# Kernel tuning notes

Measured on AMD Instinct MI355X. Metric: run time of the kernel, lower is better.

The kernel has to match this reference:

```python
import jax, jax.numpy as jnp
import numpy as np

B, N, T, OBS, ACT, M, EMB = 128, 128, 256, 512, 64, 16, 128
H = T // 2  # bi-LSTM hidden per direction
EPS = 1e-5


def _ln(x, g, b):
    mu = x.mean(-1, keepdims=True)
    var = ((x - mu) ** 2).mean(-1, keepdims=True)
    return (x - mu) / jnp.sqrt(var + EPS) * g + b


def _lstm_dir(xs, Wih, Whh, bih, bhh):
    # xs: [m, T] -> hidden states [m, H]; torch gate order i,f,g,o
    h0 = jnp.zeros(xs.shape[:-2] + (H,), xs.dtype)

    def cell(carry, x):
        h, c = carry
        z = x @ Wih.T + h @ Whh.T + bih + bhh
        i, f, g, o = jnp.split(z, 4, axis=-1)
        c = jax.nn.sigmoid(f) * c + jax.nn.sigmoid(i) * jnp.tanh(g)
        h = jax.nn.sigmoid(o) * jnp.tanh(c)
        return (h, c), h

    (_, _), hs = jax.lax.scan(cell, (h0, h0), xs)
    return hs


def setup_inputs() -> dict:
    key = jax.random.key(0)
    ks = iter(jax.random.split(key, 32))

    def lin(fi, shape):
        return jax.random.normal(next(ks), shape, jnp.float32) / float(np.sqrt(fi))

    z = lambda *s: jnp.zeros(s, jnp.float32)
    o = lambda *s: jnp.ones(s, jnp.float32)
    return dict(
        obs=jax.random.normal(next(ks), (B, N, OBS), jnp.float32),
        W1=lin(OBS, (OBS, T)), b1=z(T), g1=o(T), be1=z(T),
        W2=lin(T, (T, T)), b2=z(T), g2=o(T), be2=z(T),
        Wa1=lin(T, (T, EMB)), ba1=z(EMB),
        Wa2=lin(EMB, (EMB, EMB)), ba2=z(EMB),
        Wa3=lin(EMB, (EMB, 1)), ba3=z(1),
        Wf_ih=lin(T, (4 * H, T)), Wf_hh=lin(H, (4 * H, H)), bf_ih=z(4 * H), bf_hh=z(4 * H),
        Wb_ih=lin(T, (4 * H, T)), Wb_hh=lin(H, (4 * H, H)), bb_ih=z(4 * H), bb_hh=z(4 * H),
        W3=lin(T, (T, T)), b3=z(T), g3=o(T), be3=z(T),
        W4=lin(T, (T, ACT)), b4=z(ACT), g4=o(ACT), be4=z(ACT),
    )


def reference(obs, W1, b1, g1, be1, W2, b2, g2, be2,
              Wa1, ba1, Wa2, ba2, Wa3, ba3,
              Wf_ih, Wf_hh, bf_ih, bf_hh, Wb_ih, Wb_hh, bb_ih, bb_hh,
              W3, b3, g3, be3, W4, b4, g4, be4):
    # actor_1: Linear -> LN -> ReLU -> Linear -> LN
    h = jax.nn.relu(_ln(obs @ W1 + b1, g1, be1))
    thoughts = _ln(h @ W2 + b2, g2, be2)              # [B,N,T]

    # attention unit: 2-layer MLP + sigmoid
    a = jax.nn.relu(thoughts @ Wa1 + ba1)
    a = jax.nn.relu(a @ Wa2 + ba2)
    init_prob = jax.nn.sigmoid(a @ Wa3 + ba3)          # [B,N,1]
    is_init = init_prob[..., 0] > 0.4                  # [B,N]

    # pairwise squared distances via bmm (same expansion as torch code)
    dot = jnp.einsum('bit,bjt->bij', thoughts, thoughts)
    sq = jnp.diagonal(dot, axis1=1, axis2=2)           # [B,N]
    dists = sq[:, None, :] - 2.0 * dot + sq[:, :, None]

    # top-m nearest neighbors per agent, then agent-index order (matches j-loop order)
    _, idx = jax.lax.top_k(-dists, M)                  # [B,N,M]
    idx = jnp.sort(idx, axis=-1)

    bidx = jnp.arange(B)[:, None, None]
    aidx = jnp.arange(N)[None, :, None]
    C = jnp.zeros((B, N, N), thoughts.dtype).at[bidx, aidx, idx].set(1.0)
    C = C * is_init[..., None].astype(thoughts.dtype)

    old_thoughts = thoughts

    # sequential per-agent communication: gather group, bi-LSTM, scatter back
    def update_one(th, grp_idx, flags):
        def step(t, inp):
            gi, fl = inp
            grp = t[gi]                                 # [M,T]
            hf = _lstm_dir(grp, Wf_ih, Wf_hh, bf_ih, bf_hh)
            hb = _lstm_dir(grp[::-1], Wb_ih, Wb_hh, bb_ih, bb_hh)[::-1]
            integ = jnp.concatenate([hf, hb], -1)       # [M,T]
            t = t.at[gi].set(jnp.where(fl, integ, grp))
            return t, None
        t, _ = jax.lax.scan(step, th, (grp_idx, flags))
        return t

    new_thoughts = jax.vmap(update_one)(thoughts, idx, is_init)

    # actor_2: ReLU -> Linear -> LN -> Linear -> LN -> Tanh
    h2 = jax.nn.relu(new_thoughts)
    h2 = _ln(h2 @ W3 + b3, g3, be3)
    acts = jnp.tanh(_ln(h2 @ W4 + b4, g4, be4))
    return acts, C, init_prob, is_init, new_thoughts, old_thoughts
```

## Files before the change

kernel.cpp:

```cpp
#include <hip/hip_runtime.h>
#include <math.h>

typedef __attribute__((ext_vector_type(8))) short bf16x8;
typedef __attribute__((ext_vector_type(4))) float f32x4;

__device__ __forceinline__ unsigned short f2bf(float x) {
    unsigned int u = __float_as_uint(x);
    u += 0x7fffu + ((u >> 16) & 1u);
    return (unsigned short)(u >> 16);
}
__device__ __forceinline__ float bf2f(unsigned short b) {
    return __uint_as_float(((unsigned int)b) << 16);
}
__device__ __forceinline__ float fsig(float z) {
    float e = __expf(-z);
    return __builtin_amdgcn_rcpf(1.f + e);
}
__device__ __forceinline__ float ftanh(float x) {
    float e = __expf(-2.f * x);
    float s = __builtin_amdgcn_rcpf(1.f + e);
    return fmaf(2.f, s, -1.f);
}
__device__ __forceinline__ bf16x8 pack8(float4 a, float4 b) {
    bf16x8 r;
    r[0] = (short)f2bf(a.x); r[1] = (short)f2bf(a.y);
    r[2] = (short)f2bf(a.z); r[3] = (short)f2bf(a.w);
    r[4] = (short)f2bf(b.x); r[5] = (short)f2bf(b.y);
    r[6] = (short)f2bf(b.z); r[7] = (short)f2bf(b.w);
    return r;
}

__global__ void prep_kernel(const float* __restrict__ Wf_ih, const float* __restrict__ Wb_ih,
                            const float* __restrict__ Wf_hh, const float* __restrict__ Wb_hh,
                            const float* __restrict__ bf_ih, const float* __restrict__ bf_hh,
                            const float* __restrict__ bb_ih, const float* __restrict__ bb_hh,
                            unsigned short* __restrict__ wihbf,
                            unsigned short* __restrict__ whhbf,
                            float* __restrict__ biasz) {
    int i = blockIdx.x * 256 + threadIdx.x;
    if (i < 131072) {
        wihbf[i]          = f2bf(Wf_ih[i]);
        wihbf[131072 + i] = f2bf(Wb_ih[i]);
    }
    if (i < 65536) {
        whhbf[i]         = f2bf(Wf_hh[i]);
        whhbf[65536 + i] = f2bf(Wb_hh[i]);
    }
    if (i < 512) {
        biasz[i]       = bf_ih[i] + bf_hh[i];
        biasz[512 + i] = bb_ih[i] + bb_hh[i];
    }
}

__global__ __launch_bounds__(256) void gemm64(const float* __restrict__ A,
                                              const float* __restrict__ Bm,
                                              const float* __restrict__ bias,
                                              float* __restrict__ C,
                                              int M, int N, int K, int flags) {
    __shared__ float As[16][68];
    __shared__ float Bs[16][68];
    const int t = threadIdx.x;
    const int row0 = blockIdx.y * 64, col0 = blockIdx.x * 64;
    const int tm = t >> 4, tn = t & 15;
    float acc[4][4] = {};
    for (int k0 = 0; k0 < K; k0 += 16) {
        {
            int r = t >> 2, kq = (t & 3) * 4;
            float4 v = *(const float4*)(A + (size_t)(row0 + r) * K + k0 + kq);
            if (flags & 2) {
                v.x = fmaxf(v.x, 0.f); v.y = fmaxf(v.y, 0.f);
                v.z = fmaxf(v.z, 0.f); v.w = fmaxf(v.w, 0.f);
            }
            As[kq + 0][r] = v.x; As[kq + 1][r] = v.y;
            As[kq + 2][r] = v.z; As[kq + 3][r] = v.w;
        }
        {
            int kk = t >> 4, nq = (t & 15) * 4;
            float4 v = *(const float4*)(Bm + (size_t)(k0 + kk) * N + col0 + nq);
            *(float4*)&Bs[kk][nq] = v;
        }
        __syncthreads();
#pragma unroll
        for (int kk = 0; kk < 16; ++kk) {
            float a[4], b[4];
#pragma unroll
            for (int i = 0; i < 4; ++i) a[i] = As[kk][tm * 4 + i];
#pragma unroll
            for (int j = 0; j < 4; ++j) b[j] = Bs[kk][tn * 4 + j];
#pragma unroll
            for (int i = 0; i < 4; ++i)
#pragma unroll
                for (int j = 0; j < 4; ++j) acc[i][j] = fmaf(a[i], b[j], acc[i][j]);
        }
        __syncthreads();
    }
#pragma unroll
    for (int i = 0; i < 4; ++i) {
#pragma unroll
        for (int j = 0; j < 4; ++j) {
            int col = col0 + tn * 4 + j;
            float v = acc[i][j] + (bias ? bias[col] : 0.f);
            if (flags & 1) v = fmaxf(v, 0.f);
            C[(size_t)(row0 + tm * 4 + i) * N + col] = v;
        }
    }
}

__global__ __launch_bounds__(256) void ln256_kernel(const float* __restrict__ X,
                                                    float* __restrict__ Y,
                                                    float* __restrict__ Y2,
                                                    const float* __restrict__ gam,
                                                    const float* __restrict__ bet,
                                                    int relu) {
#pragma clang fp contract(off)
    int row = blockIdx.x * 4 + (threadIdx.x >> 6);
    int l = threadIdx.x & 63;
    float4 x = *(const float4*)(X + (size_t)row * 256 + l * 4);
    float s = x.x + x.y + x.z + x.w;
#pragma unroll
    for (int d = 1; d < 64; d <<= 1) s += __shfl_xor(s, d);
    float mu = s * (1.f / 256.f);
    float d0 = x.x - mu, d1 = x.y - mu, d2 = x.z - mu, d3 = x.w - mu;
    float ss = d0 * d0 + d1 * d1 + d2 * d2 + d3 * d3;
#pragma unroll
    for (int d = 1; d < 64; d <<= 1) ss += __shfl_xor(ss, d);
    float var = ss * (1.f / 256.f);
    float sd = sqrtf(var + 1e-5f);
    float4 y;
    y.x = (d0 / sd) * gam[l * 4 + 0] + bet[l * 4 + 0];
    y.y = (d1 / sd) * gam[l * 4 + 1] + bet[l * 4 + 1];
    y.z = (d2 / sd) * gam[l * 4 + 2] + bet[l * 4 + 2];
    y.w = (d3 / sd) * gam[l * 4 + 3] + bet[l * 4 + 3];
    if (relu) {
        y.x = fmaxf(y.x, 0.f); y.y = fmaxf(y.y, 0.f);
        y.z = fmaxf(y.z, 0.f); y.w = fmaxf(y.w, 0.f);
    }
    *(float4*)(Y + (size_t)row * 256 + l * 4) = y;
    if (Y2) *(float4*)(Y2 + (size_t)row * 256 + l * 4) = y;
}

__global__ __launch_bounds__(256) void ln64_tanh_kernel(const float* __restrict__ X,
                                                        float* __restrict__ Y,
                                                        const float* __restrict__ gam,
                                                        const float* __restrict__ bet) {
#pragma clang fp contract(off)
    int row = blockIdx.x * 4 + (threadIdx.x >> 6);
    int l = threadIdx.x & 63;
    float x = X[(size_t)row * 64 + l];
    float s = x;
#pragma unroll
    for (int d = 1; d < 64; d <<= 1) s += __shfl_xor(s, d);
    float mu = s * (1.f / 64.f);
    float dx = x - mu;
    float ss = dx * dx;
#pragma unroll
    for (int d = 1; d < 64; d <<= 1) ss += __shfl_xor(ss, d);
    float var = ss * (1.f / 64.f);
    float sd = sqrtf(var + 1e-5f);
    float y = tanhf((dx / sd) * gam[l] + bet[l]);
    Y[(size_t)row * 64 + l] = y;
}

__global__ __launch_bounds__(256) void attn_head_kernel(const float* __restrict__ a2,
                                                        const float* __restrict__ Wa3,
                                                        const float* __restrict__ ba3,
                                                        float* __restrict__ outP,
                                                        float* __restrict__ outInit,
                                                        int* __restrict__ flags) {
#pragma clang fp contract(off)
    int row = blockIdx.x * 4 + (threadIdx.x >> 6);
    int l = threadIdx.x & 63;
    float s = a2[(size_t)row * 128 + l] * Wa3[l] + a2[(size_t)row * 128 + 64 + l] * Wa3[64 + l];
#pragma unroll
    for (int d = 1; d < 64; d <<= 1) s += __shfl_xor(s, d);
    s += ba3[0];
    float p = 1.f / (1.f + expf(-s));
    if (l == 0) {
        outP[row] = p;
        int f = (p > 0.4f) ? 1 : 0;
        outInit[row] = f ? 1.f : 0.f;
        flags[row] = f;
    }
}

__global__ __launch_bounds__(256) void dot_kernel(const float* __restrict__ th,
                                                  float* __restrict__ dotm) {
    __shared__ float As[16][68];
    __shared__ float Bs[16][132];
    const int b = blockIdx.x >> 1, half = blockIdx.x & 1;
    const int t = threadIdx.x;
    const int tm = t >> 4, tn = t & 15;
    float acc[4][8] = {};
    const float* base = th + (size_t)b * 128 * 256;
    for (int k0 = 0; k0 < 256; k0 += 16) {
        {
            int r = t >> 2, kq = (t & 3) * 4;
            float4 v = *(const float4*)(base + (size_t)(half * 64 + r) * 256 + k0 + kq);
            As[kq + 0][r] = v.x; As[kq + 1][r] = v.y;
            As[kq + 2][r] = v.z; As[kq + 3][r] = v.w;
        }
        {
            int n = t >> 1, kq = (t & 1) * 8;
            const float* src = base + (size_t)n * 256 + k0 + kq;
            float4 v0 = *(const float4*)src;
            float4 v1 = *(const float4*)(src + 4);
            Bs[kq + 0][n] = v0.x; Bs[kq + 1][n] = v0.y;
            Bs[kq + 2][n] = v0.z; Bs[kq + 3][n] = v0.w;
            Bs[kq + 4][n] = v1.x; Bs[kq + 5][n] = v1.y;
            Bs[kq + 6][n] = v1.z; Bs[kq + 7][n] = v1.w;
        }
        __syncthreads();
#pragma unroll
        for (int kk = 0; kk < 16; ++kk) {
            float a[4], bb[8];
#pragma unroll
            for (int i = 0; i < 4; ++i) a[i] = As[kk][tm * 4 + i];
#pragma unroll
            for (int j = 0; j < 8; ++j) bb[j] = Bs[kk][tn * 8 + j];
#pragma unroll
            for (int i = 0; i < 4; ++i)
#pragma unroll
                for (int j = 0; j < 8; ++j) acc[i][j] = fmaf(a[i], bb[j], acc[i][j]);
        }
        __syncthreads();
    }
#pragma unroll
    for (int i = 0; i < 4; ++i)
#pragma unroll
        for (int j = 0; j < 8; ++j)
            dotm[(size_t)b * 16384 + (size_t)(half * 64 + tm * 4 + i) * 128 + tn * 8 + j] = acc[i][j];
}

__global__ void sq_kernel(const float* __restrict__ dotm, float* __restrict__ sq) {
    int i = blockIdx.x * 256 + threadIdx.x;
    int b = i >> 7, n = i & 127;
    sq[i] = dotm[(size_t)b * 16384 + (size_t)n * 129];
}

__global__ __launch_bounds__(256) void topk_kernel(const float* __restrict__ dotm,
                                                   const float* __restrict__ sq,
                                                   const int* __restrict__ flags,
                                                   float* __restrict__ outC,
                                                   int* __restrict__ idxb) {
#pragma clang fp contract(off)
    int row = blockIdx.x * 4 + (threadIdx.x >> 6);
    int l = threadIdx.x & 63;
    int b = row >> 7;
    const float* drow = dotm + (size_t)row * 128;
    float sqi = sq[row];
    float t0 = 2.f * drow[l];
    float v0 = sq[b * 128 + l] - t0; v0 = v0 + sqi;
    float t1 = 2.f * drow[64 + l];
    float v1 = sq[b * 128 + 64 + l] - t1; v1 = v1 + sqi;

    unsigned long long mlo = 0ull, mhi = 0ull;
#pragma unroll 1
    for (int n = 0; n < 16; ++n) {
        float bv = v0; int bi = l;
        if (v1 < bv) { bv = v1; bi = 64 + l; }
#pragma unroll
        for (int d = 1; d < 64; d <<= 1) {
            float ov = __shfl_xor(bv, d);
            int oi = __shfl_xor(bi, d);
            if (ov < bv || (ov == bv && oi < bi)) { bv = ov; bi = oi; }
        }
        if (bi < 64) mlo |= (1ull << bi); else mhi |= (1ull << (bi - 64));
        if (l == bi) v0 = __builtin_inff();
        if (64 + l == bi) v1 = __builtin_inff();
    }
    float fl = (flags[row] != 0) ? 1.f : 0.f;
    outC[(size_t)row * 128 + l]      = fl * (((mlo >> l) & 1ull) ? 1.f : 0.f);
    outC[(size_t)row * 128 + 64 + l] = fl * (((mhi >> l) & 1ull) ? 1.f : 0.f);
    if (l < 16) {
        int cnt = 0, found = -1;
        for (int jj = 0; jj < 128; ++jj) {
            bool bit = (jj < 64) ? ((mlo >> jj) & 1ull) : ((mhi >> (jj - 64)) & 1ull);
            if (bit) { if (cnt == l) { found = jj; break; } ++cnt; }
        }
        idxb[(size_t)row * 16 + l] = found;
    }
}

__global__ __launch_bounds__(512, 2) void chain_kernel(float* __restrict__ th,
                                                       const unsigned short* __restrict__ whhbf,
                                                       const unsigned short* __restrict__ wihbf,
                                                       const float* __restrict__ biasz,
                                                       const int* __restrict__ idxb,
                                                       const int* __restrict__ flags) {
    const int b = blockIdx.x;
    const int t = threadIdx.x;
    const int l = t & 63, lr = l & 15, lg = l >> 4;
    const int w = t >> 6, dir = w >> 2, wd = w & 3;

    __shared__ __align__(16) unsigned short thl[128 * 256];
    __shared__ __align__(16) unsigned short xgs2[2 * 4 * 16 * 16 * 8];
    __shared__ __align__(16) unsigned short hsnap[2][18][128];
    __shared__ int idxl[2048];
    __shared__ int flg[128];

    {
        int r = t >> 2, c0 = (t & 3) * 64;
        const float* src = th + (size_t)(b * 128 + r) * 256 + c0;
        char* rowb = (char*)thl + r * 512;
        int swz = (r & 7) << 4;
#pragma unroll
        for (int i = 0; i < 8; ++i) {
            float4 v0 = *(const float4*)(src + i * 8);
            float4 v1 = *(const float4*)(src + i * 8 + 4);
            *(bf16x8*)(rowb + (((c0 + i * 8) * 2) ^ swz)) = pack8(v0, v1);
        }
    }
    if (t < 128) flg[t] = flags[b * 128 + t];
    if (t < 256) {
        int d2 = t >> 7, j = t & 127;
        hsnap[d2][0][j] = 0;
        hsnap[d2][17][j] = 0;
    }
#pragma unroll
    for (int c = 0; c < 4; ++c) idxl[t + c * 512] = idxb[(size_t)b * 2048 + c * 512 + t];

    bf16x8 wf[4][2][4];
    {
        const unsigned short* whh = whhbf + (size_t)dir * 65536;
#pragma unroll
        for (int G = 0; G < 4; ++G)
#pragma unroll
            for (int hf = 0; hf < 2; ++hf) {
                int gate = G * 128 + wd * 32 + 2 * lr + hf;
#pragma unroll
                for (int kc = 0; kc < 4; ++kc)
                    wf[G][hf][kc] = *(const bf16x8*)(whh + (size_t)gate * 128 + kc * 32 + lg * 8);
            }
    }
    const unsigned short* wih = wihbf + (size_t)dir * 131072;
    float bzr[8];
#pragma unroll
    for (int tt = 0; tt < 8; ++tt)
        bzr[tt] = biasz[dir * 512 + (tt >> 1) * 128 + wd * 32 + 2 * lr + (tt & 1)];
    __syncthreads();

    for (int ag = 0; ag < 128; ++ag) {
        if (!flg[ag]) continue;
        const int gi_lr = idxl[ag * 16 + lr];
        const int xgbase = ((dir * 4 + wd) * 16) * 16 * 8;

        {
            f32x4 xa[8];
#pragma unroll
            for (int tt = 0; tt < 8; ++tt) xa[tt] = (f32x4){0.f, 0.f, 0.f, 0.f};
            const char* arow = (const char*)thl + gi_lr * 512;
            const int aswz = (gi_lr & 7) << 4;
#pragma unroll
            for (int kc = 0; kc < 8; ++kc) {
                bf16x8 af = *(const bf16x8*)(arow + ((kc * 64 + lg * 16) ^ aswz));
#pragma unroll
                for (int tt = 0; tt < 8; ++tt) {
                    const unsigned short* wb =
                        wih + (size_t)((tt >> 1) * 128 + wd * 32 + 2 * lr + (tt & 1)) * 256 +
                        kc * 32 + lg * 8;
                    xa[tt] = __builtin_amdgcn_mfma_f32_16x16x32_bf16(
                        af, *(const bf16x8*)wb, xa[tt], 0, 0, 0);
                }
            }
#pragma unroll
            for (int r = 0; r < 4; ++r) {
                bf16x8 pk;
#pragma unroll
                for (int tt = 0; tt < 8; ++tt) pk[tt] = (short)f2bf(xa[tt][r] + bzr[tt]);
                int m = lg * 4 + r;
                *(bf16x8*)&xgs2[xgbase + (m * 16 + lr) * 8] = pk;
            }
        }
        __syncthreads();

        bf16x8 xpn = *(const bf16x8*)&xgs2[xgbase + ((dir ? 15 : 0) * 16 + lr) * 8];

        float cst0 = 0.f, cst1 = 0.f;
        for (int s = 0; s < 16; ++s) {
            const int m = dir ? (15 - s) : s;
            const int rprev = dir ? (m + 2) : m;
            f32x4 acc[4][2];
#pragma unroll
            for (int G = 0; G < 4; ++G) {
                acc[G][0] = (f32x4){0.f, 0.f, 0.f, 0.f};
                acc[G][1] = (f32x4){0.f, 0.f, 0.f, 0.f};
            }
#pragma unroll
            for (int kc = 0; kc < 4; ++kc) {
                bf16x8 ha = *(const bf16x8*)(&hsnap[dir][rprev][kc * 32 + lg * 8]);
#pragma unroll
                for (int G = 0; G < 4; ++G) {
                    acc[G][0] = __builtin_amdgcn_mfma_f32_16x16x32_bf16(
                        ha, wf[G][0][kc], acc[G][0], 0, 0, 0);
                    acc[G][1] = __builtin_amdgcn_mfma_f32_16x16x32_bf16(
                        ha, wf[G][1][kc], acc[G][1], 0, 0, 0);
                }
            }
            bf16x8 xp = xpn;
            float zi0 = acc[0][0][0] + bf2f((unsigned short)xp[0]);
            float zi1 = acc[0][1][0] + bf2f((unsigned short)xp[1]);
            float zf0 = acc[1][0][0] + bf2f((unsigned short)xp[2]);
            float zf1 = acc[1][1][0] + bf2f((unsigned short)xp[3]);
            float zg0 = acc[2][0][0] + bf2f((unsigned short)xp[4]);
            float zg1 = acc[2][1][0] + bf2f((unsigned short)xp[5]);
            float zo0 = acc[3][0][0] + bf2f((unsigned short)xp[6]);
            float zo1 = acc[3][1][0] + bf2f((unsigned short)xp[7]);
            float i0 = fsig(zi0), f0 = fsig(zf0), g0 = ftanh(zg0), o0 = fsig(zo0);
            cst0 = f0 * cst0 + i0 * g0;
            float h0 = o0 * ftanh(cst0);
            float i1 = fsig(zi1), f1 = fsig(zf1), g1 = ftanh(zg1), o1 = fsig(zo1);
            cst1 = f1 * cst1 + i1 * g1;
            float h1 = o1 * ftanh(cst1);
            if (lg == 0) {
                unsigned int hw = (unsigned int)f2bf(h0) | ((unsigned int)f2bf(h1) << 16);
                *(unsigned int*)&hsnap[dir][m + 1][wd * 32 + 2 * lr] = hw;
            }
            if (s < 15) {
                int mn = dir ? (14 - s) : (s + 1);
                xpn = *(const bf16x8*)&xgs2[xgbase + (mn * 16 + lr) * 8];
            }
            __syncthreads();
        }

        {
            int d2 = t >> 8, m = (t >> 4) & 15, c8 = (t & 15) * 8;
            bf16x8 v = *(const bf16x8*)&hsnap[d2][m + 1][c8];
            int row = idxl[ag * 16 + m];
            *(bf16x8*)((char*)thl + row * 512 + (((d2 * 128 + c8) * 2) ^ ((row & 7) << 4))) = v;
        }
        __syncthreads();
    }

    {
        int r = t >> 2, c0 = (t & 3) * 64;
        const char* rowb = (const char*)thl + r * 512;
        int swz = (r & 7) << 4;
        float* dst = th + (size_t)(b * 128 + r) * 256 + c0;
#pragma unroll
        for (int i = 0; i < 8; ++i) {
            bf16x8 sv = *(const bf16x8*)(rowb + (((c0 + i * 8) * 2) ^ swz));
            float4 v0, v1;
            v0.x = bf2f((unsigned short)sv[0]); v0.y = bf2f((unsigned short)sv[1]);
            v0.z = bf2f((unsigned short)sv[2]); v0.w = bf2f((unsigned short)sv[3]);
            v1.x = bf2f((unsigned short)sv[4]); v1.y = bf2f((unsigned short)sv[5]);
            v1.z = bf2f((unsigned short)sv[6]); v1.w = bf2f((unsigned short)sv[7]);
            *(float4*)(dst + i * 8) = v0;
            *(float4*)(dst + i * 8 + 4) = v1;
        }
    }
}

extern "C" void kernel_launch(void* const* d_in, const int* in_sizes, int n_in,
                              void* d_out, int out_size, void* d_ws, size_t ws_size,
                              hipStream_t stream) {
    const float* obs  = (const float*)d_in[0];
    const float* W1   = (const float*)d_in[1];
    const float* b1   = (const float*)d_in[2];
    const float* gg1  = (const float*)d_in[3];
    const float* be1  = (const float*)d_in[4];
    const float* W2   = (const float*)d_in[5];
    const float* b2   = (const float*)d_in[6];
    const float* gg2  = (const float*)d_in[7];
    const float* be2  = (const float*)d_in[8];
    const float* Wa1  = (const float*)d_in[9];
    const float* ba1  = (const float*)d_in[10];
    const float* Wa2  = (const float*)d_in[11];
    const float* ba2  = (const float*)d_in[12];
    const float* Wa3  = (const float*)d_in[13];
    const float* ba3  = (const float*)d_in[14];
    const float* Wf_ih = (const float*)d_in[15];
    const float* Wf_hh = (const float*)d_in[16];
    const float* bf_ih = (const float*)d_in[17];
    const float* bf_hh = (const float*)d_in[18];
    const float* Wb_ih = (const float*)d_in[19];
    const float* Wb_hh = (const float*)d_in[20];
    const float* bb_ih = (const float*)d_in[21];
    const float* bb_hh = (const float*)d_in[22];
    const float* W3   = (const float*)d_in[23];
    const float* b3   = (const float*)d_in[24];
    const float* gg3  = (const float*)d_in[25];
    const float* be3  = (const float*)d_in[26];
    const float* W4   = (const float*)d_in[27];
    const float* b4   = (const float*)d_in[28];
    const float* gg4  = (const float*)d_in[29];
    const float* be4  = (const float*)d_in[30];

    float* out     = (float*)d_out;
    float* out_acts = out;
    float* out_C    = out + 1048576;
    float* out_ip   = out + 3145728;
    float* out_ii   = out + 3162112;
    float* out_nt   = out + 3178496;
    float* out_ot   = out + 7372800;

    float* ws    = (float*)d_ws;
    float* h1    = ws;
    float* abuf  = ws + 4194304;
    float* a2buf = ws + 6291456;
    unsigned short* wihbf = (unsigned short*)(ws + 8388608);
    float* biasz = ws + 8519680;
    unsigned short* whhbf = (unsigned short*)(ws + 8520704);
    float* sqb   = ws + 8586240;
    int* idxb    = (int*)(ws + 8602624);
    int* flagsb  = (int*)(ws + 8864768);

    prep_kernel<<<512, 256, 0, stream>>>(Wf_ih, Wb_ih, Wf_hh, Wb_hh,
                                         bf_ih, bf_hh, bb_ih, bb_hh,
                                         wihbf, whhbf, biasz);

    gemm64<<<dim3(4, 256), 256, 0, stream>>>(obs, W1, b1, h1, 16384, 256, 512, 0);
    ln256_kernel<<<4096, 256, 0, stream>>>(h1, h1, nullptr, gg1, be1, 1);
    gemm64<<<dim3(4, 256), 256, 0, stream>>>(h1, W2, b2, out_nt, 16384, 256, 256, 0);
    ln256_kernel<<<4096, 256, 0, stream>>>(out_nt, out_nt, out_ot, gg2, be2, 0);

    gemm64<<<dim3(2, 256), 256, 0, stream>>>(out_nt, Wa1, ba1, abuf, 16384, 128, 256, 1);
    gemm64<<<dim3(2, 256), 256, 0, stream>>>(abuf, Wa2, ba2, a2buf, 16384, 128, 128, 1);
    attn_head_kernel<<<4096, 256, 0, stream>>>(a2buf, Wa3, ba3, out_ip, out_ii, flagsb);

    dot_kernel<<<256, 256, 0, stream>>>(out_nt, abuf);
    sq_kernel<<<64, 256, 0, stream>>>(abuf, sqb);
    topk_kernel<<<4096, 256, 0, stream>>>(abuf, sqb, flagsb, out_C, idxb);

    chain_kernel<<<128, 512, 0, stream>>>(out_nt, whhbf, wihbf, biasz, idxb, flagsb);

    gemm64<<<dim3(4, 256), 256, 0, stream>>>(out_nt, W3, b3, h1, 16384, 256, 256, 2);
    ln256_kernel<<<4096, 256, 0, stream>>>(h1, h1, nullptr, gg3, be3, 0);
    gemm64<<<dim3(1, 256), 256, 0, stream>>>(h1, W4, b4, a2buf, 16384, 64, 256, 0);
    ln64_tanh_kernel<<<4096, 256, 0, stream>>>(a2buf, out_acts, gg4, be4);
}
```

Baseline: 3.612 ms.

## Interleave two batches per chain block and move thought state to global bf16

The chain kernel now processes two batch elements per workgroup, running 64 blocks instead of 128. The two independent LSTM recurrences are interleaved so their MFMA and transcendental latencies can overlap. The per-batch thought matrix no longer lives in LDS. A separate kernel converts it to a global bf16 copy, which is read for the input projection and written back together with fp32 updates. The biases and input gates are folded into the accumulator initialisation. The trade-off is half as many blocks, which halves the parallelism across CUs, plus global-memory latency on the gather path.

Result: slower. 7.664 ms (+112.2%).

```diff
diff --git a/kernel.cpp b/kernel.cpp
--- a/kernel.cpp
+++ b/kernel.cpp
@@ -50,6 +50,13 @@
         biasz[i]       = bf_ih[i] + bf_hh[i];
         biasz[512 + i] = bb_ih[i] + bb_hh[i];
     }
+}
+
+__global__ void tobf_kernel(const float* __restrict__ x, unsigned short* __restrict__ y) {
+    int i = (blockIdx.x * 256 + threadIdx.x) * 8;
+    float4 v0 = *(const float4*)(x + i);
+    float4 v1 = *(const float4*)(x + i + 4);
+    *(bf16x8*)(y + i) = pack8(v0, v1);
 }
 
 __global__ __launch_bounds__(256) void gemm64(const float* __restrict__ A,
@@ -282,42 +289,36 @@
 }
 
 __global__ __launch_bounds__(512, 2) void chain_kernel(float* __restrict__ th,
+                                                       unsigned short* __restrict__ thbf,
                                                        const unsigned short* __restrict__ whhbf,
                                                        const unsigned short* __restrict__ wihbf,
                                                        const float* __restrict__ biasz,
                                                        const int* __restrict__ idxb,
                                                        const int* __restrict__ flags) {
-    const int b = blockIdx.x;
+    const int blk = blockIdx.x;
     const int t = threadIdx.x;
     const int l = t & 63, lr = l & 15, lg = l >> 4;
     const int w = t >> 6, dir = w >> 2, wd = w & 3;
 
-    __shared__ __align__(16) unsigned short thl[128 * 256];
-    __shared__ __align__(16) unsigned short xgs2[2 * 4 * 16 * 16 * 8];
-    __shared__ __align__(16) unsigned short hsnap[2][18][128];
-    __shared__ int idxl[2048];
-    __shared__ int flg[128];
-
-    {
-        int r = t >> 2, c0 = (t & 3) * 64;
-        const float* src = th + (size_t)(b * 128 + r) * 256 + c0;
-        char* rowb = (char*)thl + r * 512;
-        int swz = (r & 7) << 4;
-#pragma unroll
-        for (int i = 0; i < 8; ++i) {
-            float4 v0 = *(const float4*)(src + i * 8);
-            float4 v1 = *(const float4*)(src + i * 8 + 4);
-            *(bf16x8*)(rowb + (((c0 + i * 8) * 2) ^ swz)) = pack8(v0, v1);
-        }
-    }
-    if (t < 128) flg[t] = flags[b * 128 + t];
+    __shared__ __align__(16) unsigned short xgs2[2][16384];
+    __shared__ __align__(16) unsigned short hsnap[2][2][18][128];
+    __shared__ int idxl[2][2048];
+    __shared__ int flg[2][128];
+
+    if (t < 128) {
+        flg[0][t] = flags[(blk * 2) * 128 + t];
+        flg[1][t] = flags[(blk * 2 + 1) * 128 + t];
+    }
     if (t < 256) {
-        int d2 = t >> 7, j = t & 127;
-        hsnap[d2][0][j] = 0;
-        hsnap[d2][17][j] = 0;
-    }
-#pragma unroll
-    for (int c = 0; c < 4; ++c) idxl[t + c * 512] = idxb[(size_t)b * 2048 + c * 512 + t];
+        int bb = t >> 7, j = t & 127;
+        hsnap[bb][0][0][j] = 0; hsnap[bb][0][17][j] = 0;
+        hsnap[bb][1][0][j] = 0; hsnap[bb][1][17][j] = 0;
+    }
+#pragma unroll
+    for (int c = 0; c < 4; ++c) {
+        idxl[0][c * 512 + t] = idxb[(size_t)(blk * 2) * 2048 + c * 512 + t];
+        idxl[1][c * 512 + t] = idxb[(size_t)(blk * 2 + 1) * 2048 + c * 512 + t];
+    }
 
     bf16x8 wf[4][2][4];
     {
@@ -339,20 +340,24 @@
         bzr[tt] = biasz[dir * 512 + (tt >> 1) * 128 + wd * 32 + 2 * lr + (tt & 1)];
     __syncthreads();
 
+    const int xgoff = ((dir * 4 + wd) * 16) * 128;
+
     for (int ag = 0; ag < 128; ++ag) {
-        if (!flg[ag]) continue;
-        const int gi_lr = idxl[ag * 16 + lr];
-        const int xgbase = ((dir * 4 + wd) * 16) * 16 * 8;
-
-        {
+        const int a0 = flg[0][ag], a1 = flg[1][ag];
+        if (!(a0 | a1)) continue;
+
+#pragma unroll
+        for (int bb = 0; bb < 2; ++bb) {
+            if (!(bb ? a1 : a0)) continue;
+            int gi = idxl[bb][ag * 16 + lr];
+            const unsigned short* arow = thbf + (size_t)((blk * 2 + bb) * 128 + gi) * 256;
             f32x4 xa[8];
 #pragma unroll
-            for (int tt = 0; tt < 8; ++tt) xa[tt] = (f32x4){0.f, 0.f, 0.f, 0.f};
-            const char* arow = (const char*)thl + gi_lr * 512;
-            const int aswz = (gi_lr & 7) << 4;
+            for (int tt = 0; tt < 8; ++tt)
+                xa[tt] = (f32x4){bzr[tt], bzr[tt], bzr[tt], bzr[tt]};
 #pragma unroll
             for (int kc = 0; kc < 8; ++kc) {
-                bf16x8 af = *(const bf16x8*)(arow + ((kc * 64 + lg * 16) ^ aswz));
+                bf16x8 af = *(const bf16x8*)(arow + kc * 32 + lg * 8);
 #pragma unroll
                 for (int tt = 0; tt < 8; ++tt) {
                     const unsigned short* wb =
@@ -366,87 +371,113 @@
             for (int r = 0; r < 4; ++r) {
                 bf16x8 pk;
 #pragma unroll
-                for (int tt = 0; tt < 8; ++tt) pk[tt] = (short)f2bf(xa[tt][r] + bzr[tt]);
+                for (int tt = 0; tt < 8; ++tt) pk[tt] = (short)f2bf(xa[tt][r]);
                 int m = lg * 4 + r;
-                *(bf16x8*)&xgs2[xgbase + (m * 16 + lr) * 8] = pk;
+                *(bf16x8*)&xgs2[bb][xgoff + (m * 16 + lr) * 8] = pk;
             }
         }
         __syncthreads();
 
-        bf16x8 xpn = *(const bf16x8*)&xgs2[xgbase + ((dir ? 15 : 0) * 16 + lr) * 8];
-
-        float cst0 = 0.f, cst1 = 0.f;
+        bf16x8 xp0, xp1;
+        const int m0 = dir ? 15 : 0;
+        if (a0) xp0 = *(const bf16x8*)&xgs2[0][xgoff + (m0 * 16 + lr) * 8];
+        if (a1) xp1 = *(const bf16x8*)&xgs2[1][xgoff + (m0 * 16 + lr) * 8];
+        float c00 = 0.f, c01 = 0.f, c10 = 0.f, c11 = 0.f;
+
         for (int s = 0; s < 16; ++s) {
             const int m = dir ? (15 - s) : s;
             const int rprev = dir ? (m + 2) : m;
-            f32x4 acc[4][2];
-#pragma unroll
-            for (int G = 0; G < 4; ++G) {
-                acc[G][0] = (f32x4){0.f, 0.f, 0.f, 0.f};
-                acc[G][1] = (f32x4){0.f, 0.f, 0.f, 0.f};
-            }
-#pragma unroll
-            for (int kc = 0; kc < 4; ++kc) {
-                bf16x8 ha = *(const bf16x8*)(&hsnap[dir][rprev][kc * 32 + lg * 8]);
-#pragma unroll
-                for (int G = 0; G < 4; ++G) {
-                    acc[G][0] = __builtin_amdgcn_mfma_f32_16x16x32_bf16(
-                        ha, wf[G][0][kc], acc[G][0], 0, 0, 0);
-                    acc[G][1] = __builtin_amdgcn_mfma_f32_16x16x32_bf16(
-                        ha, wf[G][1][kc], acc[G][1], 0, 0, 0);
+            const int mn = dir ? (14 - s) : (s + 1);
+            if (a0) {
+                f32x4 acc[4][2];
+#pragma unroll
+                for (int G = 0; G < 4; ++G)
+#pragma unroll
+                    for (int hf = 0; hf < 2; ++hf) {
+                        float xv = bf2f((unsigned short)xp0[G * 2 + hf]);
+                        acc[G][hf] = (f32x4){xv, xv, xv, xv};
+                    }
+#pragma unroll
+                for (int kc = 0; kc < 4; ++kc) {
+                    bf16x8 ha = *(const bf16x8*)(&hsnap[0][dir][rprev][kc * 32 + lg * 8]);
+#pragma unroll
+                    for (int G = 0; G < 4; ++G) {
+                        acc[G][0] = __builtin_amdgcn_mfma_f32_16x16x32_bf16(
+                            ha, wf[G][0][kc], acc[G][0], 0, 0, 0);
+                        acc[G][1] = __builtin_amdgcn_mfma_f32_16x16x32_bf16(
+                            ha, wf[G][1][kc], acc[G][1], 0, 0, 0);
+                    }
                 }
-            }
-            bf16x8 xp = xpn;
-            float zi0 = acc[0][0][0] + bf2f((unsigned short)xp[0]);
-            float zi1 = acc[0][1][0] + bf2f((unsigned short)xp[1]);
-            float zf0 = acc[1][0][0] + bf2f((unsigned short)xp[2]);
-            float zf1 = acc[1][1][0] + bf2f((unsigned short)xp[3]);
-            float zg0 = acc[2][0][0] + bf2f((unsigned short)xp[4]);
-            float zg1 = acc[2][1][0] + bf2f((unsigned short)xp[5]);
-            float zo0 = acc[3][0][0] + bf2f((unsigned short)xp[6]);
-            float zo1 = acc[3][1][0] + bf2f((unsigned short)xp[7]);
-            float i0 = fsig(zi0), f0 = fsig(zf0), g0 = ftanh(zg0), o0 = fsig(zo0);
-            cst0 = f0 * cst0 + i0 * g0;
-            float h0 = o0 * ftanh(cst0);
-            float i1 = fsig(zi1), f1 = fsig(zf1), g1 = ftanh(zg1), o1 = fsig(zo1);
-            cst1 = f1 * cst1 + i1 * g1;
-            float h1 = o1 * ftanh(cst1);
-            if (lg == 0) {
-                unsigned int hw = (unsigned int)f2bf(h0) | ((unsigned int)f2bf(h1) << 16);
-                *(unsigned int*)&hsnap[dir][m + 1][wd * 32 + 2 * lr] = hw;
-            }
-            if (s < 15) {
-                int mn = dir ? (14 - s) : (s + 1);
-                xpn = *(const bf16x8*)&xgs2[xgbase + (mn * 16 + lr) * 8];
+                float i0 = fsig(acc[0][0][0]), f0 = fsig(acc[1][0][0]);
+                float g0 = ftanh(acc[2][0][0]), o0 = fsig(acc[3][0][0]);
+                c00 = f0 * c00 + i0 * g0;
+                float h0 = o0 * ftanh(c00);
+                float i1 = fsig(acc[0][1][0]), f1 = fsig(acc[1][1][0]);
+                float g1 = ftanh(acc[2][1][0]), o1 = fsig(acc[3][1][0]);
+                c01 = f1 * c01 + i1 * g1;
+                float h1 = o1 * ftanh(c01);
+                if (lg == 0) {
+                    unsigned int hw = (unsigned int)f2bf(h0) | ((unsigned int)f2bf(h1) << 16);
+                    *(unsigned int*)&hsnap[0][dir][m + 1][wd * 32 + 2 * lr] = hw;
+                }
+                if (s < 15) xp0 = *(const bf16x8*)&xgs2[0][xgoff + (mn * 16 + lr) * 8];
+            }
+            if (a1) {
+                f32x4 acc[4][2];
+#pragma unroll
+                for (int G = 0; G < 4; ++G)
+#pragma unroll
+                    for (int hf = 0; hf < 2; ++hf) {
+                        float xv = bf2f((unsigned short)xp1[G * 2 + hf]);
+                        acc[G][hf] = (f32x4){xv, xv, xv, xv};
+                    }
+#pragma unroll
+                for (int kc = 0; kc < 4; ++kc) {
+                    bf16x8 ha = *(const bf16x8*)(&hsnap[1][dir][rprev][kc * 32 + lg * 8]);
+#pragma unroll
+                    for (int G = 0; G < 4; ++G) {
+                        acc[G][0] = __builtin_amdgcn_mfma_f32_16x16x32_bf16(
+                            ha, wf[G][0][kc], acc[G][0], 0, 0, 0);
+                        acc[G][1] = __builtin_amdgcn_mfma_f32_16x16x32_bf16(
+                            ha, wf[G][1][kc], acc[G][1], 0, 0, 0);
+                    }
+                }
+                float i0 = fsig(acc[0][0][0]), f0 = fsig(acc[1][0][0]);
+                float g0 = ftanh(acc[2][0][0]), o0 = fsig(acc[3][0][0]);
+                c10 = f0 * c10 + i0 * g0;
+                float h0 = o0 * ftanh(c10);
+                float i1 = fsig(acc[0][1][0]), f1 = fsig(acc[1][1][0]);
+                float g1 = ftanh(acc[2][1][0]), o1 = fsig(acc[3][1][0]);
+                c11 = f1 * c11 + i1 * g1;
+                float h1 = o1 * ftanh(c11);
+                if (lg == 0) {
+                    unsigned int hw = (unsigned int)f2bf(h0) | ((unsigned int)f2bf(h1) << 16);
+                    *(unsigned int*)&hsnap[1][dir][m + 1][wd * 32 + 2 * lr] = hw;
+                }
+                if (s < 15) xp1 = *(const bf16x8*)&xgs2[1][xgoff + (mn * 16 + lr) * 8];
             }
             __syncthreads();
         }
 
         {
-            int d2 = t >> 8, m = (t >> 4) & 15, c8 = (t & 15) * 8;
-            bf16x8 v = *(const bf16x8*)&hsnap[d2][m + 1][c8];
-            int row = idxl[ag * 16 + m];
-            *(bf16x8*)((char*)thl + row * 512 + (((d2 * 128 + c8) * 2) ^ ((row & 7) << 4))) = v;
+            int d2 = t >> 8, mm = (t >> 4) & 15, c8 = (t & 15) * 8;
+#pragma unroll
+            for (int bb = 0; bb < 2; ++bb) {
+                if (!(bb ? a1 : a0)) continue;
+                bf16x8 v = *(const bf16x8*)&hsnap[bb][d2][mm + 1][c8];
+                int row = idxl[bb][ag * 16 + mm];
+                size_t base = (size_t)((blk * 2 + bb) * 128 + row) * 256 + d2 * 128 + c8;
+                *(bf16x8*)(thbf + base) = v;
+                float4 f0, f1;
+                f0.x = bf2f((unsigned short)v[0]); f0.y = bf2f((unsigned short)v[1]);
+                f0.z = bf2f((unsigned short)v[2]); f0.w = bf2f((unsigned short)v[3]);
+                f1.x = bf2f((unsigned short)v[4]); f1.y = bf2f((unsigned short)v[5]);
+                f1.z = bf2f((unsigned short)v[6]); f1.w = bf2f((unsigned short)v[7]);
+                *(float4*)(th + base) = f0;
+                *(float4*)(th + base + 4) = f1;
+            }
         }
         __syncthreads();
-    }
-
-    {
-        int r = t >> 2, c0 = (t & 3) * 64;
-        const char* rowb = (const char*)thl + r * 512;
-        int swz = (r & 7) << 4;
-        float* dst = th + (size_t)(b * 128 + r) * 256 + c0;
-#pragma unroll
-        for (int i = 0; i < 8; ++i) {
-            bf16x8 sv = *(const bf16x8*)(rowb + (((c0 + i * 8) * 2) ^ swz));
-            float4 v0, v1;
-            v0.x = bf2f((unsigned short)sv[0]); v0.y = bf2f((unsigned short)sv[1]);
-            v0.z = bf2f((unsigned short)sv[2]); v0.w = bf2f((unsigned short)sv[3]);
-            v1.x = bf2f((unsigned short)sv[4]); v1.y = bf2f((unsigned short)sv[5]);
-            v1.z = bf2f((unsigned short)sv[6]); v1.w = bf2f((unsigned short)sv[7]);
-            *(float4*)(dst + i * 8) = v0;
-            *(float4*)(dst + i * 8 + 4) = v1;
-        }
     }
 }
 
@@ -503,6 +534,7 @@
     float* sqb   = ws + 8586240;
     int* idxb    = (int*)(ws + 8602624);
     int* flagsb  = (int*)(ws + 8864768);
+    unsigned short* thbf = (unsigned short*)a2buf;
 
     prep_kernel<<<512, 256, 0, stream>>>(Wf_ih, Wb_ih, Wf_hh, Wb_hh,
                                          bf_ih, bf_hh, bb_ih, bb_hh,
@@ -521,7 +553,9 @@
     sq_kernel<<<64, 256, 0, stream>>>(abuf, sqb);
     topk_kernel<<<4096, 256, 0, stream>>>(abuf, sqb, flagsb, out_C, idxb);
 
-    chain_kernel<<<128, 512, 0, stream>>>(out_nt, whhbf, wihbf, biasz, idxb, flagsb);
+    tobf_kernel<<<2048, 256, 0, stream>>>(out_nt, thbf);
+
+    chain_kernel<<<64, 512, 0, stream>>>(out_nt, thbf, whhbf, wihbf, biasz, idxb, flagsb);
 
     gemm64<<<dim3(4, 256), 256, 0, stream>>>(out_nt, W3, b3, h1, 16384, 256, 256, 2);
     ln256_kernel<<<4096, 256, 0, stream>>>(h1, h1, nullptr, gg3, be3, 0);
```
